# Kernel optimization log

Measured on AMD Instinct MI355X. Metric: run time of the kernel, lower is better.

The kernel has to match this reference:

```python
import jax, jax.numpy as jnp
import numpy as np

H = 16  # num_heads


def setup_inputs() -> dict:
    key = jax.random.key(0)
    ks = jax.random.split(key, 12)
    B, T, D, E = 2, 2048, 1024, 16384
    s = 0.02
    return {
        "x": jax.random.normal(ks[0], (B, T, D), jnp.float32),
        "Wq": jax.random.normal(ks[1], (D, D), jnp.float32) * s,
        "bq": jnp.zeros((D,), jnp.float32),
        "Wk": jax.random.normal(ks[2], (D, D), jnp.float32) * s,
        "bk": jnp.zeros((D,), jnp.float32),
        "Wv": jax.random.normal(ks[3], (D, D), jnp.float32) * s,
        "bv": jnp.zeros((D,), jnp.float32),
        "Wo": jax.random.normal(ks[4], (D, D), jnp.float32) * s,
        "bo": jnp.zeros((D,), jnp.float32),
        "edge_emb": jax.random.normal(ks[5], (3, D), jnp.float32) * s,  # TypedEdgeEmbedding table
        "type_w": jax.random.normal(ks[6], (D,), jnp.float32) * s,      # type_to_bias Linear(D,1,bias=False)
        "edge_src": jax.random.randint(ks[7], (E,), 0, T, jnp.int32),
        "edge_dst": jax.random.randint(ks[8], (E,), 0, T, jnp.int32),
        "edge_types": jax.random.randint(ks[9], (E,), 0, 3, jnp.int32),
    }


def reference(x, Wq, bq, Wk, bk, Wv, bv, Wo, bo, edge_emb, type_w,
              edge_src, edge_dst, edge_types):
    B, T, D = x.shape
    hd = D // H
    scale = 1.0 / jnp.sqrt(jnp.float32(hd))
    # QKV projections -> [B, H, T, hd]
    q = (x @ Wq + bq).reshape(B, T, H, hd).transpose(0, 2, 1, 3)
    k = (x @ Wk + bk).reshape(B, T, H, hd).transpose(0, 2, 1, 3)
    v = (x @ Wv + bv).reshape(B, T, H, hd).transpose(0, 2, 1, 3)
    # dense attention scores [B, H, T, T]
    scores = jnp.einsum('bhqd,bhkd->bhqk', q, k) * scale
    # typed edge bias: emb lookup -> linear to scalar per edge; same across B, H
    bias_e = edge_emb[edge_types] @ type_w  # [E]
    # scatter-add bias into scores at (src, dst) for every batch/head
    scores = scores.at[:, :, edge_src, edge_dst].add(bias_e)
    attn = jax.nn.softmax(scores, axis=-1)  # dropout is identity in eval / p=0
    out = jnp.einsum('bhqk,bhkd->bhqd', attn, v)
    out = out.transpose(0, 2, 1, 3).reshape(B, T, D)
    return out @ Wo + bo
```

## Files before the change

### kernel.cpp

```cpp
#include <hip/hip_runtime.h>


typedef __attribute__((ext_vector_type(4))) float f32x4;
typedef __attribute__((ext_vector_type(16))) float f32x16;
typedef __bf16 bf16x8 __attribute__((ext_vector_type(8)));

#define DEV static __device__ __forceinline__

DEV ushort f2bf(float f) {
  unsigned u = __float_as_uint(f);
  unsigned r = u + 0x7fffu + ((u >> 16) & 1u);
  return (ushort)(r >> 16);
}

DEV float bf2f(ushort u) { return __uint_as_float((unsigned)u << 16); }

DEV void gl_lds16(const void* g, void* l) {
  __builtin_amdgcn_global_load_lds(
      (const __attribute__((address_space(1))) void*)g,
      (__attribute__((address_space(3))) void*)l, 16, 0, 0);
}

DEV f32x16 mfma32(bf16x8 a, bf16x8 b, f32x16 c) {
  return __builtin_amdgcn_mfma_f32_32x32x16_bf16(a, b, c, 0, 0, 0);
}

DEV unsigned cvtpk(float a, float b) {
  unsigned r;
  asm("v_cvt_pk_bf16_f32 %0, %1, %2" : "=v"(r) : "v"(a), "v"(b));
  return r;
}

__global__ __launch_bounds__(256) void cvtx_kernel(const float* __restrict__ X,
                                                   ushort* __restrict__ Y) {
  int i = blockIdx.x * 256 + threadIdx.x;
  float4 v = ((const float4*)X)[i];
  ushort4 o;
  o.x = f2bf(v.x); o.y = f2bf(v.y); o.z = f2bf(v.z); o.w = f2bf(v.w);
  ((ushort4*)Y)[i] = o;
}

__global__ __launch_bounds__(256) void tcvt_kernel(const float* __restrict__ W,
                                                   ushort* __restrict__ Wt) {
  __shared__ float tile[32][33];
  int bx = blockIdx.x * 32, by = blockIdx.y * 32;
  int tx = threadIdx.x & 31, ty = threadIdx.x >> 5;
#pragma unroll
  for (int i = 0; i < 32; i += 8)
    tile[ty + i][tx] = W[(size_t)(by + ty + i) * 1024 + bx + tx];
  __syncthreads();
#pragma unroll
  for (int i = 0; i < 32; i += 8)
    Wt[(size_t)(bx + ty + i) * 1024 + by + tx] = f2bf(tile[tx][ty + i]);
}

__global__ __launch_bounds__(256) void bias3_kernel(const float* __restrict__ emb,
                                                    const float* __restrict__ tw,
                                                    float* __restrict__ b3) {
  __shared__ float red[256];
  const int t = blockIdx.x;
  float p = 0.f;
  for (int d = threadIdx.x; d < 1024; d += 256) p += emb[t * 1024 + d] * tw[d];
  red[threadIdx.x] = p;
  __syncthreads();
  for (int s = 128; s > 0; s >>= 1) {
    if (threadIdx.x < s) red[threadIdx.x] += red[threadIdx.x + s];
    __syncthreads();
  }
  if (threadIdx.x == 0) b3[t] = red[0];
}

__global__ __launch_bounds__(256) void scatterT_kernel(
    const int* __restrict__ src, const int* __restrict__ dst,
    const int* __restrict__ typ, const float* __restrict__ b3,
    float* __restrict__ BiasT, int E) {
  int e = blockIdx.x * 256 + threadIdx.x;
  if (e < E) atomicAdd(&BiasT[(size_t)dst[e] * 2048 + src[e]], b3[typ[e]]);
}

__global__ __launch_bounds__(256) void dexpT_kernel(const float* __restrict__ B,
                                                    ushort* __restrict__ D) {
  int i = blockIdx.x * 256 + threadIdx.x;
  f32x4 v = ((const f32x4*)B)[i];
  ushort4 o;
#pragma unroll
  for (int j = 0; j < 4; ++j) ((ushort*)&o)[j] = f2bf(__expf(v[j]) - 1.0f);
  ((ushort4*)D)[i] = o;
}

__global__ __launch_bounds__(256) void gemm_qkv_kernel(
    const ushort* __restrict__ A, const ushort* __restrict__ Bt3,
    const float* __restrict__ bq, const float* __restrict__ bk,
    const float* __restrict__ bv, ushort* __restrict__ Qo,
    ushort* __restrict__ Ko, ushort* __restrict__ Vto) {
  __shared__ alignas(16) char Als[16384];
  __shared__ alignas(16) char Bls[16384];
  const int tid = threadIdx.x, w = tid >> 6, l = tid & 63;
  const int m0 = blockIdx.y * 128, n0 = blockIdx.x * 128;
  const int sr = l >> 2, sg = l & 3;
  const int c = l & 15, gg = l >> 4;
  const int wr = (w >> 1) * 64, wc = (w & 1) * 64;

  f32x4 acc[4][4];
  const f32x4 zf = {0.f, 0.f, 0.f, 0.f};
#pragma unroll
  for (int a2 = 0; a2 < 4; ++a2)
#pragma unroll
    for (int b2 = 0; b2 < 4; ++b2) acc[a2][b2] = zf;

  for (int k0 = 0; k0 < 1024; k0 += 64) {
#pragma unroll
    for (int j = 0; j < 4; ++j) {
      const int idx = w * 4 + j, kk = idx >> 3, mb = idx & 7;
      gl_lds16(A + (size_t)(m0 + mb * 16 + sr) * 1024 + k0 + kk * 32 + sg * 8,
               &Als[idx * 1024]);
      gl_lds16(Bt3 + (size_t)(n0 + mb * 16 + sr) * 1024 + k0 + kk * 32 + sg * 8,
               &Bls[idx * 1024]);
    }
    __syncthreads();
#pragma unroll
    for (int kk = 0; kk < 2; ++kk) {
      bf16x8 af[4], bfr[4];
#pragma unroll
      for (int f = 0; f < 4; ++f) {
        af[f]  = *(const bf16x8*)&Als[(kk * 8 + (wr >> 4) + f) * 1024 + c * 64 + gg * 16];
        bfr[f] = *(const bf16x8*)&Bls[(kk * 8 + (wc >> 4) + f) * 1024 + c * 64 + gg * 16];
      }
#pragma unroll
      for (int mf = 0; mf < 4; ++mf)
#pragma unroll
        for (int nf = 0; nf < 4; ++nf)
          acc[mf][nf] = __builtin_amdgcn_mfma_f32_16x16x32_bf16(
              af[mf], bfr[nf], acc[mf][nf], 0, 0, 0);
    }
    __syncthreads();
  }

  const int which = n0 >> 10;
  const float scale = (which == 0) ? 0.125f : 1.0f;
  const float* bias = (which == 0) ? bq : (which == 1) ? bk : bv;
  ushort* outp = (which == 0) ? Qo : (which == 1) ? Ko : Vto;
#pragma unroll
  for (int mf = 0; mf < 4; ++mf) {
#pragma unroll
    for (int nf = 0; nf < 4; ++nf) {
      const int coln = (n0 & 1023) + wc + nf * 16 + c;
      const float bvv = bias[coln];
      const int h = coln >> 6, d = coln & 63;
#pragma unroll
      for (int i = 0; i < 4; ++i) {
        const int row = m0 + wr + mf * 16 + gg * 4 + i;
        const int b = row >> 11, t = row & 2047;
        const float v = (acc[mf][nf][i] + bvv) * scale;
        if (which < 2)
          outp[((size_t)(b * 16 + h) * 2048 + t) * 64 + d] = f2bf(v);
        else
          outp[((size_t)(b * 16 + h) * 64 + d) * 2048 + t] = f2bf(v);
      }
    }
  }
}

__global__ __launch_bounds__(256) void gemm_out_kernel(
    const ushort* __restrict__ A, const ushort* __restrict__ Bt,
    const float* __restrict__ bias, float* __restrict__ outp) {
  __shared__ alignas(16) char Als[16384];
  __shared__ alignas(16) char Bls[16384];
  const int tid = threadIdx.x, w = tid >> 6, l = tid & 63;
  const int m0 = blockIdx.y * 128, n0 = blockIdx.x * 128;
  const int sr = l >> 2, sg = l & 3;
  const int c = l & 15, gg = l >> 4;
  const int wr = (w >> 1) * 64, wc = (w & 1) * 64;

  f32x4 acc[4][4];
  const f32x4 zf = {0.f, 0.f, 0.f, 0.f};
#pragma unroll
  for (int a2 = 0; a2 < 4; ++a2)
#pragma unroll
    for (int b2 = 0; b2 < 4; ++b2) acc[a2][b2] = zf;

  for (int k0 = 0; k0 < 1024; k0 += 64) {
#pragma unroll
    for (int j = 0; j < 4; ++j) {
      const int idx = w * 4 + j, kk = idx >> 3, mb = idx & 7;
      gl_lds16(A + (size_t)(m0 + mb * 16 + sr) * 1024 + k0 + kk * 32 + sg * 8,
               &Als[idx * 1024]);
      gl_lds16(Bt + (size_t)(n0 + mb * 16 + sr) * 1024 + k0 + kk * 32 + sg * 8,
               &Bls[idx * 1024]);
    }
    __syncthreads();
#pragma unroll
    for (int kk = 0; kk < 2; ++kk) {
      bf16x8 af[4], bfr[4];
#pragma unroll
      for (int f = 0; f < 4; ++f) {
        af[f]  = *(const bf16x8*)&Als[(kk * 8 + (wr >> 4) + f) * 1024 + c * 64 + gg * 16];
        bfr[f] = *(const bf16x8*)&Bls[(kk * 8 + (wc >> 4) + f) * 1024 + c * 64 + gg * 16];
      }
#pragma unroll
      for (int mf = 0; mf < 4; ++mf)
#pragma unroll
        for (int nf = 0; nf < 4; ++nf)
          acc[mf][nf] = __builtin_amdgcn_mfma_f32_16x16x32_bf16(
              af[mf], bfr[nf], acc[mf][nf], 0, 0, 0);
    }
    __syncthreads();
  }

#pragma unroll
  for (int mf = 0; mf < 4; ++mf) {
#pragma unroll
    for (int nf = 0; nf < 4; ++nf) {
      const int col = n0 + wc + nf * 16 + c;
      const float bvv = bias[col];
#pragma unroll
      for (int i = 0; i < 4; ++i) {
        const int row = m0 + wr + mf * 16 + gg * 4 + i;
        outp[(size_t)row * 1024 + col] = acc[mf][nf][i] + bvv;
      }
    }
  }
}

__global__ __launch_bounds__(512, 4) void attn5_kernel(
    const ushort* __restrict__ Q, const ushort* __restrict__ K,
    const ushort* __restrict__ Vt, const ushort* __restrict__ DT,
    ushort* __restrict__ Out) {
  __shared__ alignas(16) char smem[65536];
  const int tid = threadIdx.x, w = tid >> 6, l = tid & 63;
  const int c = l & 31, hi = l >> 5;
  const int bid = blockIdx.x;
  const int bh = (bid & 7) * 4 + ((bid >> 3) & 3);
  const int qt = bid >> 5;
  const int bI = bh >> 4, h = bh & 15;
  const int qd = w >> 2, ww = w & 3;
  const int qw = qt * 128 + ww * 32;
  const int kq = qd * 1024;
  const int qsb = qd * 32768;
  const char* Kg = (const char*)(K + (size_t)bh * 2048 * 64);
  const char* Vg = (const char*)(Vt + (size_t)bh * 64 * 2048);

  const ushort* Qp = Q + ((size_t)bh * 2048 + qw + c) * 64 + hi * 8;
  bf16x8 Qf[4];
#pragma unroll
  for (int ds = 0; ds < 4; ++ds) Qf[ds] = *(const bf16x8*)(Qp + ds * 16);

  const int srb = ww * 8 + (l >> 3);
  const int scol = ((l & 7) << 4) ^ ((l >> 3) << 4);
  const int cx = (c & 7) << 4;

  f32x16 oacc0 = {0,0,0,0,0,0,0,0,0,0,0,0,0,0,0,0};
  f32x16 oacc1 = {0,0,0,0,0,0,0,0,0,0,0,0,0,0,0,0};
  float l_run = 0.f;

  auto STAGE = [&](int buf, int t0) {
#pragma unroll
    for (int j = 0; j < 2; ++j) {
      const int r = j * 32 + srb;
      gl_lds16(Kg + (size_t)(kq + t0 + r) * 128 + scol,
               &smem[qsb + buf * 8192 + j * 4096 + ww * 1024]);
      gl_lds16(Vg + (size_t)r * 4096 + (size_t)(kq + t0) * 2 + scol,
               &smem[qsb + 16384 + buf * 8192 + j * 4096 + ww * 1024]);
    }
  };

  STAGE(0, 0);
  for (int t = 0; t < 16; ++t) {
    const int cur = t & 1;
    __syncthreads();
    if (t < 15) STAGE(cur ^ 1, (t + 1) * 64);
    const char* KsC = smem + qsb + cur * 8192;
    const char* VsC = smem + qsb + 16384 + cur * 8192;

    f32x16 s0 = {0,0,0,0,0,0,0,0,0,0,0,0,0,0,0,0};
    f32x16 s1 = {0,0,0,0,0,0,0,0,0,0,0,0,0,0,0,0};
#pragma unroll
    for (int ds = 0; ds < 4; ++ds) {
      const int col = (ds * 32 + hi * 16) ^ cx;
      bf16x8 k0 = *(const bf16x8*)(KsC + c * 128 + col);
      bf16x8 k1 = *(const bf16x8*)(KsC + (32 + c) * 128 + col);
      s0 = mfma32(k0, Qf[ds], s0);
      s1 = mfma32(k1, Qf[ds], s1);
    }

    const ushort* bp = DT + ((size_t)(kq + t * 64 + 4 * hi)) * 2048 + qw + c;
    float ps[16];
#pragma unroll
    for (int r = 0; r < 16; ++r) {
      const int off = ((r & 3) + 8 * (r >> 2)) * 2048;
      const float d0 = bf2f(bp[off]);
      const float d1 = bf2f(bp[off + 65536]);
      float p0 = __expf(s0[r] - 3.0f);
      float p1 = __expf(s1[r] - 3.0f);
      p0 = fmaf(p0, d0, p0);
      p1 = fmaf(p1, d1, p1);
      s0[r] = p0; s1[r] = p1;
      ps[r] = p0 + p1;
    }
#pragma unroll
    for (int off = 8; off; off >>= 1)
#pragma unroll
      for (int r = 0; r < off; ++r) ps[r] += ps[r + off];
    l_run += ps[0];

    bf16x8 paf[2][2];
#pragma unroll
    for (int kt = 0; kt < 2; ++kt) {
      const f32x16& sv = kt ? s1 : s0;
#pragma unroll
      for (int sl = 0; sl < 2; ++sl) {
        const int rb = sl * 8;
        unsigned u0 = cvtpk(sv[rb + 0], sv[rb + 1]);
        unsigned u1 = cvtpk(sv[rb + 2], sv[rb + 3]);
        unsigned u2 = cvtpk(sv[rb + 4], sv[rb + 5]);
        unsigned u3 = cvtpk(sv[rb + 6], sv[rb + 7]);
        asm("v_permlane32_swap_b32 %0, %1" : "+v"(u0), "+v"(u2));
        asm("v_permlane32_swap_b32 %0, %1" : "+v"(u1), "+v"(u3));
        uint4 uu = {u0, u1, u2, u3};
        paf[kt][sl] = *(bf16x8*)&uu;
      }
    }

#pragma unroll
    for (int kt = 0; kt < 2; ++kt)
#pragma unroll
      for (int sl = 0; sl < 2; ++sl) {
        const int ks = kt * 2 + sl;
        const int col = (ks * 32 + hi * 16) ^ cx;
        bf16x8 v0 = *(const bf16x8*)(VsC + c * 128 + col);
        bf16x8 v1 = *(const bf16x8*)(VsC + (32 + c) * 128 + col);
        oacc0 = mfma32(paf[kt][sl], v0, oacc0);
        oacc1 = mfma32(paf[kt][sl], v1, oacc1);
      }
  }

  __syncthreads();
  const float l_tot = l_run + __shfl_xor(l_run, 32);
  float* mb  = (float*)smem + ww * 2048;
  float* lb  = (float*)(smem + 32768);
  float* lb2 = (float*)(smem + 32768 + 512);
  if (qd == 1) {
#pragma unroll
    for (int r = 0; r < 16; ++r) {
      const int qr = (r & 3) + 8 * (r >> 2) + 4 * hi;
      mb[qr * 64 + c] = oacc0[r];
      mb[qr * 64 + 32 + c] = oacc1[r];
    }
    lb[ww * 32 + c] = l_tot;
  }
  __syncthreads();
  if (qd == 0) {
    const float linv = 1.0f / (l_tot + lb[ww * 32 + c]);
    lb2[ww * 32 + c] = linv;
    const float* lp = lb2 + ww * 32 + hi * 4;
    f32x4 lv[4];
#pragma unroll
    for (int g2 = 0; g2 < 4; ++g2) lv[g2] = *(const f32x4*)(lp + 8 * g2);
    ushort* Ob = Out + ((size_t)bI * 2048 + qw) * 1024 + h * 64;
#pragma unroll
    for (int r = 0; r < 16; ++r) {
      const int qr = (r & 3) + 8 * (r >> 2) + 4 * hi;
      const float sc = lv[r >> 2][r & 3];
      const float o0 = (oacc0[r] + mb[qr * 64 + c]) * sc;
      const float o1 = (oacc1[r] + mb[qr * 64 + 32 + c]) * sc;
      Ob[(size_t)qr * 1024 + c] = f2bf(o0);
      Ob[(size_t)qr * 1024 + 32 + c] = f2bf(o1);
    }
  }
}

extern "C" void kernel_launch(void* const* d_in, const int* in_sizes, int n_in,
                              void* d_out, int out_size, void* d_ws, size_t ws_size,
                              hipStream_t stream) {
  (void)n_in; (void)out_size; (void)ws_size;
  const float* x   = (const float*)d_in[0];
  const float* Wq  = (const float*)d_in[1];
  const float* bq  = (const float*)d_in[2];
  const float* Wk  = (const float*)d_in[3];
  const float* bk  = (const float*)d_in[4];
  const float* Wv  = (const float*)d_in[5];
  const float* bv  = (const float*)d_in[6];
  const float* Wo  = (const float*)d_in[7];
  const float* bo  = (const float*)d_in[8];
  const float* emb = (const float*)d_in[9];
  const float* tw  = (const float*)d_in[10];
  const int* esrc  = (const int*)d_in[11];
  const int* edst  = (const int*)d_in[12];
  const int* etyp  = (const int*)d_in[13];
  const int E = in_sizes[11];

  char* ws = (char*)d_ws;
  const size_t MB = 1u << 20;
  ushort* Wtq = (ushort*)(ws + 0 * MB);
  ushort* Wtk = (ushort*)(ws + 2 * MB);
  ushort* Wtv = (ushort*)(ws + 4 * MB);
  ushort* Wto = (ushort*)(ws + 6 * MB);
  ushort* Wt3 = Wtq;
  ushort* Qb  = (ushort*)(ws + 8 * MB);
  ushort* Kb  = (ushort*)(ws + 16 * MB);
  ushort* Vtb = (ushort*)(ws + 24 * MB);
  ushort* Ab  = (ushort*)(ws + 32 * MB);
  float*  BiasT = (float*)(ws + 40 * MB);
  float*  b3   = (float*)(ws + 56 * MB);
  ushort* xbf = (ushort*)d_out;
  ushort* DT  = (ushort*)((char*)d_out + 8388608);

  cvtx_kernel<<<4096, 256, 0, stream>>>(x, xbf);
  dim3 tg(32, 32);
  tcvt_kernel<<<tg, 256, 0, stream>>>(Wq, Wtq);
  tcvt_kernel<<<tg, 256, 0, stream>>>(Wk, Wtk);
  tcvt_kernel<<<tg, 256, 0, stream>>>(Wv, Wtv);
  tcvt_kernel<<<tg, 256, 0, stream>>>(Wo, Wto);
  bias3_kernel<<<3, 256, 0, stream>>>(emb, tw, b3);
  (void)hipMemsetAsync(BiasT, 0, (size_t)2048 * 2048 * 4, stream);
  scatterT_kernel<<<(E + 255) / 256, 256, 0, stream>>>(esrc, edst, etyp, b3,
                                                       BiasT, E);
  dexpT_kernel<<<4096, 256, 0, stream>>>(BiasT, DT);

  dim3 gqkv(24, 32);
  gemm_qkv_kernel<<<gqkv, 256, 0, stream>>>(xbf, Wt3, bq, bk, bv, Qb, Kb, Vtb);
  attn5_kernel<<<512, 512, 0, stream>>>(Qb, Kb, Vtb, DT, Ab);
  dim3 go(8, 32);
  gemm_out_kernel<<<go, 256, 0, stream>>>(Ab, Wto, bo, (float*)d_out);
}
```

Baseline: 172.5 us.

## Retile out-GEMM, swizzle GEMM grids, repack bias layout, use exp2 with folded scale

The per-edge bias matrix is repacked so each lane fetches four consecutive key entries with one vector load, and those loads are issued early into registers ahead of the score MFMAs. Softmax uses a native exp2, with log2(e) folded into the Q scale and the max offset folded into the MFMA accumulator init, which removes a subtract per element. The output GEMM switches to 64x128 tiles to double the block count, and both GEMMs use a swizzled linear block index to improve L2 reuse. The four weight transpose launches are merged into one. These changes add register pressure in the attention loop and a strided read in the bias repack kernel.

```diff
diff --git a/kernel.cpp b/kernel.cpp
--- a/kernel.cpp
+++ b/kernel.cpp
@@ -6,6 +6,9 @@
 typedef __bf16 bf16x8 __attribute__((ext_vector_type(8)));
 
 #define DEV static __device__ __forceinline__
+
+#define QSCALE 0.18033688011112042f
+#define SINIT -4.328085122666891f
 
 DEV ushort f2bf(float f) {
   unsigned u = __float_as_uint(f);
@@ -14,6 +17,14 @@
 }
 
 DEV float bf2f(ushort u) { return __uint_as_float((unsigned)u << 16); }
+
+DEV float fexp2(float x) {
+#if __has_builtin(__builtin_amdgcn_exp2f)
+  return __builtin_amdgcn_exp2f(x);
+#else
+  return exp2f(x);
+#endif
+}
 
 DEV void gl_lds16(const void* g, void* l) {
   __builtin_amdgcn_global_load_lds(
@@ -40,9 +51,14 @@
   ((ushort4*)Y)[i] = o;
 }
 
-__global__ __launch_bounds__(256) void tcvt_kernel(const float* __restrict__ W,
-                                                   ushort* __restrict__ Wt) {
+__global__ __launch_bounds__(256) void tcvt4_kernel(
+    const float* __restrict__ W0, const float* __restrict__ W1,
+    const float* __restrict__ W2, const float* __restrict__ W3,
+    ushort* __restrict__ Wt) {
   __shared__ float tile[32][33];
+  const int z = blockIdx.z;
+  const float* W = (z == 0) ? W0 : (z == 1) ? W1 : (z == 2) ? W2 : W3;
+  ushort* dst = Wt + (size_t)z * 1048576;
   int bx = blockIdx.x * 32, by = blockIdx.y * 32;
   int tx = threadIdx.x & 31, ty = threadIdx.x >> 5;
 #pragma unroll
@@ -51,7 +67,7 @@
   __syncthreads();
 #pragma unroll
   for (int i = 0; i < 32; i += 8)
-    Wt[(size_t)(bx + ty + i) * 1024 + by + tx] = f2bf(tile[tx][ty + i]);
+    dst[(size_t)(bx + ty + i) * 1024 + by + tx] = f2bf(tile[tx][ty + i]);
 }
 
 __global__ __launch_bounds__(256) void bias3_kernel(const float* __restrict__ emb,
@@ -78,14 +94,17 @@
   if (e < E) atomicAdd(&BiasT[(size_t)dst[e] * 2048 + src[e]], b3[typ[e]]);
 }
 
-__global__ __launch_bounds__(256) void dexpT_kernel(const float* __restrict__ B,
-                                                    ushort* __restrict__ D) {
-  int i = blockIdx.x * 256 + threadIdx.x;
-  f32x4 v = ((const f32x4*)B)[i];
+__global__ __launch_bounds__(256) void dexpT2_kernel(const float* __restrict__ B,
+                                                     ushort* __restrict__ D) {
+  const int idx = blockIdx.x * 256 + threadIdx.x;
+  const int q = idx & 2047, kg = idx >> 11;
   ushort4 o;
 #pragma unroll
-  for (int j = 0; j < 4; ++j) ((ushort*)&o)[j] = f2bf(__expf(v[j]) - 1.0f);
-  ((ushort4*)D)[i] = o;
+  for (int j = 0; j < 4; ++j) {
+    const float v = B[(size_t)(kg * 4 + j) * 2048 + q];
+    ((ushort*)&o)[j] = f2bf(__expf(v) - 1.0f);
+  }
+  *(ushort4*)(D + ((size_t)kg * 2048 + q) * 4) = o;
 }
 
 __global__ __launch_bounds__(256) void gemm_qkv_kernel(
@@ -96,7 +115,9 @@
   __shared__ alignas(16) char Als[16384];
   __shared__ alignas(16) char Bls[16384];
   const int tid = threadIdx.x, w = tid >> 6, l = tid & 63;
-  const int m0 = blockIdx.y * 128, n0 = blockIdx.x * 128;
+  const int lin = blockIdx.x;
+  const int swz = (lin & 7) * 96 + (lin >> 3);
+  const int m0 = (swz / 24) * 128, n0 = (swz % 24) * 128;
   const int sr = l >> 2, sg = l & 3;
   const int c = l & 15, gg = l >> 4;
   const int wr = (w >> 1) * 64, wc = (w & 1) * 64;
@@ -137,7 +158,7 @@
   }
 
   const int which = n0 >> 10;
-  const float scale = (which == 0) ? 0.125f : 1.0f;
+  const float scale = (which == 0) ? QSCALE : 1.0f;
   const float* bias = (which == 0) ? bq : (which == 1) ? bk : bv;
   ushort* outp = (which == 0) ? Qo : (which == 1) ? Ko : Vto;
 #pragma unroll
@@ -164,41 +185,48 @@
 __global__ __launch_bounds__(256) void gemm_out_kernel(
     const ushort* __restrict__ A, const ushort* __restrict__ Bt,
     const float* __restrict__ bias, float* __restrict__ outp) {
-  __shared__ alignas(16) char Als[16384];
+  __shared__ alignas(16) char Als[8192];
   __shared__ alignas(16) char Bls[16384];
   const int tid = threadIdx.x, w = tid >> 6, l = tid & 63;
-  const int m0 = blockIdx.y * 128, n0 = blockIdx.x * 128;
+  const int lin = blockIdx.x;
+  const int swz = (lin & 7) * 64 + (lin >> 3);
+  const int m0 = (swz >> 3) * 64, n0 = (swz & 7) * 128;
   const int sr = l >> 2, sg = l & 3;
   const int c = l & 15, gg = l >> 4;
-  const int wr = (w >> 1) * 64, wc = (w & 1) * 64;
-
-  f32x4 acc[4][4];
+  const int wr = (w & 1) * 32, wc = (w >> 1) * 64;
+
+  f32x4 acc[2][4];
   const f32x4 zf = {0.f, 0.f, 0.f, 0.f};
 #pragma unroll
-  for (int a2 = 0; a2 < 4; ++a2)
+  for (int a2 = 0; a2 < 2; ++a2)
 #pragma unroll
     for (int b2 = 0; b2 < 4; ++b2) acc[a2][b2] = zf;
 
   for (int k0 = 0; k0 < 1024; k0 += 64) {
+#pragma unroll
+    for (int j = 0; j < 2; ++j) {
+      const int idx = w * 2 + j, kk = idx >> 2, mb = idx & 3;
+      gl_lds16(A + (size_t)(m0 + mb * 16 + sr) * 1024 + k0 + kk * 32 + sg * 8,
+               &Als[idx * 1024]);
+    }
 #pragma unroll
     for (int j = 0; j < 4; ++j) {
       const int idx = w * 4 + j, kk = idx >> 3, mb = idx & 7;
-      gl_lds16(A + (size_t)(m0 + mb * 16 + sr) * 1024 + k0 + kk * 32 + sg * 8,
-               &Als[idx * 1024]);
       gl_lds16(Bt + (size_t)(n0 + mb * 16 + sr) * 1024 + k0 + kk * 32 + sg * 8,
                &Bls[idx * 1024]);
     }
     __syncthreads();
 #pragma unroll
     for (int kk = 0; kk < 2; ++kk) {
-      bf16x8 af[4], bfr[4];
-#pragma unroll
-      for (int f = 0; f < 4; ++f) {
-        af[f]  = *(const bf16x8*)&Als[(kk * 8 + (wr >> 4) + f) * 1024 + c * 64 + gg * 16];
+      bf16x8 af[2], bfr[4];
+#pragma unroll
+      for (int f = 0; f < 2; ++f)
+        af[f] = *(const bf16x8*)&Als[(kk * 4 + (wr >> 4) + f) * 1024 + c * 64 + gg * 16];
+#pragma unroll
+      for (int f = 0; f < 4; ++f)
         bfr[f] = *(const bf16x8*)&Bls[(kk * 8 + (wc >> 4) + f) * 1024 + c * 64 + gg * 16];
-      }
-#pragma unroll
-      for (int mf = 0; mf < 4; ++mf)
+#pragma unroll
+      for (int mf = 0; mf < 2; ++mf)
 #pragma unroll
         for (int nf = 0; nf < 4; ++nf)
           acc[mf][nf] = __builtin_amdgcn_mfma_f32_16x16x32_bf16(
@@ -208,7 +236,7 @@
   }
 
 #pragma unroll
-  for (int mf = 0; mf < 4; ++mf) {
+  for (int mf = 0; mf < 2; ++mf) {
 #pragma unroll
     for (int nf = 0; nf < 4; ++nf) {
       const int col = n0 + wc + nf * 16 + c;
@@ -222,9 +250,9 @@
   }
 }
 
-__global__ __launch_bounds__(512, 4) void attn5_kernel(
+__global__ __launch_bounds__(512, 4) void attn6_kernel(
     const ushort* __restrict__ Q, const ushort* __restrict__ K,
-    const ushort* __restrict__ Vt, const ushort* __restrict__ DT,
+    const ushort* __restrict__ Vt, const ushort* __restrict__ DT2,
     ushort* __restrict__ Out) {
   __shared__ alignas(16) char smem[65536];
   const int tid = threadIdx.x, w = tid >> 6, l = tid & 63;
@@ -249,8 +277,12 @@
   const int scol = ((l & 7) << 4) ^ ((l >> 3) << 4);
   const int cx = (c & 7) << 4;
 
+  const ushort* Dbase = DT2 + ((size_t)((kq) >> 2) * 2048 + qw + c) * 4;
+
   f32x16 oacc0 = {0,0,0,0,0,0,0,0,0,0,0,0,0,0,0,0};
   f32x16 oacc1 = {0,0,0,0,0,0,0,0,0,0,0,0,0,0,0,0};
+  const f32x16 sinit = {SINIT,SINIT,SINIT,SINIT,SINIT,SINIT,SINIT,SINIT,
+                        SINIT,SINIT,SINIT,SINIT,SINIT,SINIT,SINIT,SINIT};
   float l_run = 0.f;
 
   auto STAGE = [&](int buf, int t0) {
@@ -268,12 +300,21 @@
   for (int t = 0; t < 16; ++t) {
     const int cur = t & 1;
     __syncthreads();
+
+    ushort4 dreg[8];
+    const ushort* dp = Dbase + (size_t)t * 16 * 8192;
+#pragma unroll
+    for (int j = 0; j < 4; ++j) {
+      dreg[j]     = *(const ushort4*)(dp + (size_t)(2 * j + hi) * 8192);
+      dreg[4 + j] = *(const ushort4*)(dp + (size_t)(8 + 2 * j + hi) * 8192);
+    }
+
     if (t < 15) STAGE(cur ^ 1, (t + 1) * 64);
     const char* KsC = smem + qsb + cur * 8192;
     const char* VsC = smem + qsb + 16384 + cur * 8192;
 
-    f32x16 s0 = {0,0,0,0,0,0,0,0,0,0,0,0,0,0,0,0};
-    f32x16 s1 = {0,0,0,0,0,0,0,0,0,0,0,0,0,0,0,0};
+    f32x16 s0 = sinit;
+    f32x16 s1 = sinit;
 #pragma unroll
     for (int ds = 0; ds < 4; ++ds) {
       const int col = (ds * 32 + hi * 16) ^ cx;
@@ -283,15 +324,13 @@
       s1 = mfma32(k1, Qf[ds], s1);
     }
 
-    const ushort* bp = DT + ((size_t)(kq + t * 64 + 4 * hi)) * 2048 + qw + c;
     float ps[16];
 #pragma unroll
     for (int r = 0; r < 16; ++r) {
-      const int off = ((r & 3) + 8 * (r >> 2)) * 2048;
-      const float d0 = bf2f(bp[off]);
-      const float d1 = bf2f(bp[off + 65536]);
-      float p0 = __expf(s0[r] - 3.0f);
-      float p1 = __expf(s1[r] - 3.0f);
+      const float d0 = bf2f(((const ushort*)&dreg[r >> 2])[r & 3]);
+      const float d1 = bf2f(((const ushort*)&dreg[4 + (r >> 2)])[r & 3]);
+      float p0 = fexp2(s0[r]);
+      float p1 = fexp2(s1[r]);
       p0 = fmaf(p0, d0, p0);
       p1 = fmaf(p1, d1, p1);
       s0[r] = p0; s1[r] = p1;
@@ -392,8 +431,6 @@
   char* ws = (char*)d_ws;
   const size_t MB = 1u << 20;
   ushort* Wtq = (ushort*)(ws + 0 * MB);
-  ushort* Wtk = (ushort*)(ws + 2 * MB);
-  ushort* Wtv = (ushort*)(ws + 4 * MB);
   ushort* Wto = (ushort*)(ws + 6 * MB);
   ushort* Wt3 = Wtq;
   ushort* Qb  = (ushort*)(ws + 8 * MB);
@@ -403,23 +440,18 @@
   float*  BiasT = (float*)(ws + 40 * MB);
   float*  b3   = (float*)(ws + 56 * MB);
   ushort* xbf = (ushort*)d_out;
-  ushort* DT  = (ushort*)((char*)d_out + 8388608);
+  ushort* DT2 = (ushort*)((char*)d_out + 8388608);
 
   cvtx_kernel<<<4096, 256, 0, stream>>>(x, xbf);
-  dim3 tg(32, 32);
-  tcvt_kernel<<<tg, 256, 0, stream>>>(Wq, Wtq);
-  tcvt_kernel<<<tg, 256, 0, stream>>>(Wk, Wtk);
-  tcvt_kernel<<<tg, 256, 0, stream>>>(Wv, Wtv);
-  tcvt_kernel<<<tg, 256, 0, stream>>>(Wo, Wto);
+  dim3 tg(32, 32, 4);
+  tcvt4_kernel<<<tg, 256, 0, stream>>>(Wq, Wk, Wv, Wo, Wtq);
   bias3_kernel<<<3, 256, 0, stream>>>(emb, tw, b3);
   (void)hipMemsetAsync(BiasT, 0, (size_t)2048 * 2048 * 4, stream);
   scatterT_kernel<<<(E + 255) / 256, 256, 0, stream>>>(esrc, edst, etyp, b3,
                                                        BiasT, E);
-  dexpT_kernel<<<4096, 256, 0, stream>>>(BiasT, DT);
-
-  dim3 gqkv(24, 32);
-  gemm_qkv_kernel<<<gqkv, 256, 0, stream>>>(xbf, Wt3, bq, bk, bv, Qb, Kb, Vtb);
-  attn5_kernel<<<512, 512, 0, stream>>>(Qb, Kb, Vtb, DT, Ab);
-  dim3 go(8, 32);
-  gemm_out_kernel<<<go, 256, 0, stream>>>(Ab, Wto, bo, (float*)d_out);
-}
+  dexpT2_kernel<<<4096, 256, 0, stream>>>(BiasT, DT2);
+
+  gemm_qkv_kernel<<<768, 256, 0, stream>>>(xbf, Wt3, bq, bk, bv, Qb, Kb, Vtb);
+  attn6_kernel<<<512, 512, 0, stream>>>(Qb, Kb, Vtb, DT2, Ab);
+  gemm_out_kernel<<<512, 256, 0, stream>>>(Ab, Wto, bo, (float*)d_out);
+}
```

After: 168.7 us. 1.02x faster.
